# Kernel tuning notes

Measured on AMD Instinct MI355X. Metric: run time of the kernel, lower is better.

## Reference

```python
import jax, jax.numpy as jnp
import numpy as np

D_MODEL = 1024
NHEAD = 16
HEAD_DIM = D_MODEL // NHEAD
SF_THRESHOLD = 4.0
SF_LEVELS = 8
STEP = SF_THRESHOLD / SF_LEVELS  # quantization step of ScaleAndFireNeuron
EPS = 1e-6


def setup_inputs() -> dict:
    key = jax.random.key(0)
    ks = jax.random.split(key, 12)
    B, L, D = 2, 2048, D_MODEL
    s = 1.0 / np.sqrt(D)
    inp = {
        "x": jax.random.normal(ks[0], (B, L, D), dtype=jnp.float32),
        "wq": jax.random.normal(ks[1], (D, D), dtype=jnp.float32) * s,
        "bq": jnp.zeros((D,), dtype=jnp.float32),
        "wk": jax.random.normal(ks[2], (D, D), dtype=jnp.float32) * s,
        "bk": jnp.zeros((D,), dtype=jnp.float32),
        "wv": jax.random.normal(ks[3], (D, D), dtype=jnp.float32) * s,
        "bv": jnp.zeros((D,), dtype=jnp.float32),
        "wo": jax.random.normal(ks[4], (D, D), dtype=jnp.float32) * s,
        "bo": jnp.zeros((D,), dtype=jnp.float32),
        "gq": jnp.ones((HEAD_DIM,), dtype=jnp.float32),  # SpikingQKNorm gain (q)
        "gk": jnp.ones((HEAD_DIM,), dtype=jnp.float32),  # SpikingQKNorm gain (k)
    }
    return inp


def _rms_norm(t, g):
    # SpikingQKNorm: RMS normalization over head_dim with learned gain
    return t * jax.lax.rsqrt(jnp.mean(t * t, axis=-1, keepdims=True) + EPS) * g


def _sfn(t):
    # ScaleAndFireNeuron: T=1 multi-level spike quantization with straight-through estimator.
    # Levels are integer multiples of STEP, clipped to +/- SF_LEVELS.
    q = jnp.clip(jnp.round(t / STEP), -SF_LEVELS, SF_LEVELS) * STEP
    return t + jax.lax.stop_gradient(q - t)


def reference(x, wq, bq, wk, bk, wv, bv, wo, bo, gq, gk):
    B, L, D = x.shape
    H, Dh = NHEAD, HEAD_DIM
    scale = Dh ** -0.5

    def proj(w, b):
        return (x @ w.T + b).reshape(B, L, H, Dh).transpose(0, 2, 1, 3)  # [B,H,L,Dh]

    q = _sfn(_rms_norm(proj(wq, bq), gq))
    k = _sfn(_rms_norm(proj(wk, bk), gk))
    v = _sfn(proj(wv, bv))

    scores = jnp.einsum('bhqd,bhkd->bhqk', q, k) * scale  # [B,H,L,L]
    probs = jax.nn.softmax(scores, axis=-1)
    out = jnp.einsum('bhqk,bhkd->bhqd', probs, v)  # [B,H,L,Dh]
    out = out.transpose(0, 2, 1, 3).reshape(B, L, D)
    return out @ wo.T + bo
```

## Files before the change

### kernel.cpp

```cpp
#include <hip/hip_runtime.h>
#include <stdint.h>

#define D_MODEL 1024
#define NHEAD 16
#define HEAD_DIM 64
#define SEQ 2048
#define BATCH 2
#define MROWS (BATCH*SEQ)
#define KVBLK 64
#define KVTILES (SEQ/KVBLK)

typedef unsigned short u16;
typedef short bf16x8 __attribute__((ext_vector_type(8)));
typedef float f32x4 __attribute__((ext_vector_type(4)));
typedef float f32x16 __attribute__((ext_vector_type(16)));

__device__ inline float bf2f(u16 h){ return __uint_as_float(((unsigned)h)<<16); }
__device__ inline u16 f2bf(float x){
  unsigned u = __float_as_uint(x);
  unsigned r = (u + 0x7FFFu + ((u>>16)&1u)) >> 16;
  return (u16)r;
}

__device__ inline f32x4 mfma_bf16(bf16x8 a, bf16x8 b, f32x4 c){
  return __builtin_amdgcn_mfma_f32_16x16x32_bf16(a, b, c, 0, 0, 0);
}
__device__ inline f32x16 mfma32_bf16(bf16x8 a, bf16x8 b, f32x16 c){
  return __builtin_amdgcn_mfma_f32_32x32x16_bf16(a, b, c, 0, 0, 0);
}

__device__ inline void gld_lds16(const u16* g, u16* l){
  __builtin_amdgcn_global_load_lds(
      (const __attribute__((address_space(1))) void*)g,
      (__attribute__((address_space(3))) void*)l, 16, 0, 0);
}

__device__ inline int swz8(int row){ return (row ^ (row >> 3)) & 7; }

__device__ inline uint32_t pack_bf2(float p0, float p1){
  uint32_t u0 = __float_as_uint(p0) + 0x8000u;
  uint32_t u1 = __float_as_uint(p1) + 0x8000u;
  return __builtin_amdgcn_perm(u1, u0, 0x07060302u);
}

__global__ __launch_bounds__(256) void pack_split(const float* __restrict__ src,
                                                  u16* __restrict__ hi, u16* __restrict__ lo, int n4){
  int i = blockIdx.x*256 + threadIdx.x;
  if (i >= n4) return;
  float4 v = ((const float4*)src)[i];
  float vv[4] = {v.x, v.y, v.z, v.w};
  u16 h[4], l[4];
  #pragma unroll
  for (int j=0;j<4;j++){
    h[j] = f2bf(vv[j]);
    l[j] = f2bf(vv[j] - bf2f(h[j]));
  }
  ((ushort4*)hi)[i] = make_ushort4(h[0],h[1],h[2],h[3]);
  ((ushort4*)lo)[i] = make_ushort4(l[0],l[1],l[2],l[3]);
}

__global__ __launch_bounds__(256) void pack_bias(const float* __restrict__ bq, const float* __restrict__ bk,
                                                 const float* __restrict__ bv, float* __restrict__ out){
  int i = blockIdx.x*256 + threadIdx.x;
  if (i < 1024) out[i] = bq[i];
  else if (i < 2048) out[i] = bk[i-1024];
  else if (i < 3072) out[i] = bv[i-2048];
}

template<int PHASES, int MODE>
__global__ __launch_bounds__(256) void gemm_bt(
    const u16* __restrict__ a_hi, const u16* __restrict__ a_lo,
    const u16* __restrict__ b_hi, const u16* __restrict__ b_lo,
    const float* __restrict__ bias,
    float* __restrict__ out_f,
    u16* __restrict__ qb, u16* __restrict__ kb, u16* __restrict__ vb,
    const float* __restrict__ gq, const float* __restrict__ gk,
    int M, int N, int K)
{
  __shared__ u16 lds[2][8192];
  const int tid = threadIdx.x;
  const int lane = tid & 63;
  const int w = tid >> 6;
  const int wr = w >> 1, wc = w & 1;
  const int m0 = blockIdx.x * 128;
  const int n0 = blockIdx.y * 128;
  const int KS = K / 32;
  const int NT = PHASES * KS;

  f32x4 acc[4][4];
  #pragma unroll
  for (int i=0;i<4;i++)
    #pragma unroll
    for (int j=0;j<4;j++) acc[i][j] = (f32x4){0.f,0.f,0.f,0.f};

  auto stage = [&](int buf, int kt){
    int ph = (PHASES==1) ? 0 : (kt / KS);
    int kk = (PHASES==1 ? kt : (kt % KS)) * 32;
    const u16* As = (ph==1) ? a_lo : a_hi;
    const u16* Bs = (ph==2) ? b_lo : b_hi;
    u16* base = &lds[buf][0];
    #pragma unroll
    for (int r=0;r<2;r++){
      const u16* g = As + (size_t)(m0 + (tid>>2) + r*64)*K + kk + (tid&3)*8;
      gld_lds16(g, base + w*512 + r*2048);
    }
    #pragma unroll
    for (int r=0;r<2;r++){
      const u16* g = Bs + (size_t)(n0 + (tid>>2) + r*64)*K + kk + (tid&3)*8;
      gld_lds16(g, base + 4096 + w*512 + r*2048);
    }
  };

  auto compute = [&](int buf){
    const u16* la = &lds[buf][0];
    const u16* lb = &lds[buf][4096];
    const int koff = (lane>>4)*8;
    const int rowa = wr*64 + (lane&15);
    const int rowb = wc*64 + (lane&15);
    bf16x8 af[4], bfv[4];
    #pragma unroll
    for (int i=0;i<4;i++) af[i]  = *(const bf16x8*)&la[(rowa + i*16)*32 + koff];
    #pragma unroll
    for (int i=0;i<4;i++) bfv[i] = *(const bf16x8*)&lb[(rowb + i*16)*32 + koff];
    #pragma unroll
    for (int i=0;i<4;i++)
      #pragma unroll
      for (int j=0;j<4;j++)
        acc[i][j] = mfma_bf16(af[i], bfv[j], acc[i][j]);
  };

  stage(0, 0);
  for (int kt=0; kt<NT; ++kt){
    __syncthreads();
    if (kt+1 < NT) stage((kt+1)&1, kt+1);
    compute(kt&1);
  }

  const int gcolbase = n0 + wc*64;
  if (MODE == 0){
    #pragma unroll
    for (int j=0;j<4;j++){
      float bj = bias ? bias[gcolbase + j*16 + (lane&15)] : 0.f;
      #pragma unroll
      for (int i=0;i<4;i++){
        int row = m0 + wr*64 + i*16 + (lane>>4)*4;
        #pragma unroll
        for (int r=0;r<4;r++)
          out_f[(size_t)(row+r)*N + gcolbase + j*16 + (lane&15)] = acc[i][j][r] + bj;
      }
    }
  } else {
    const int sidx = gcolbase >> 6;
    const int ttype = sidx < 16 ? 0 : (sidx < 32 ? 1 : 2);
    u16* dst = ttype==0 ? qb : (ttype==1 ? kb : vb);
    const int h = sidx - (ttype==1 ? 16 : (ttype==2 ? 32 : 0));
    float gvals[4], bvals[4];
    #pragma unroll
    for (int j=0;j<4;j++){
      int dh = j*16 + (lane&15);
      bvals[j] = bias[gcolbase + dh];
      gvals[j] = ttype==0 ? gq[dh] : (ttype==1 ? gk[dh] : 1.0f);
    }
    #pragma unroll
    for (int i=0;i<4;i++){
      #pragma unroll
      for (int r=0;r<4;r++){
        float tv[4];
        float ssq = 0.f;
        #pragma unroll
        for (int j=0;j<4;j++){ tv[j] = acc[i][j][r] + bvals[j]; ssq += tv[j]*tv[j]; }
        ssq += __shfl_xor(ssq, 1);
        ssq += __shfl_xor(ssq, 2);
        ssq += __shfl_xor(ssq, 4);
        ssq += __shfl_xor(ssq, 8);
        float s = 1.0f;
        if (ttype < 2) s = 1.0f / sqrtf(ssq * (1.0f/64.0f) + 1e-6f);
        int row = m0 + wr*64 + i*16 + (lane>>4)*4 + r;
        int bi = row >> 11, li = row & 2047;
        size_t obase = ((size_t)(bi*NHEAD + h)*SEQ + li)*HEAD_DIM;
        #pragma unroll
        for (int j=0;j<4;j++){
          float val = tv[j] * s * gvals[j];
          float z = rintf(val * 2.0f);
          z = fminf(8.0f, fmaxf(-8.0f, z));
          dst[obase + j*16 + (lane&15)] = f2bf(z * 0.5f);
        }
      }
    }
  }
}

__global__ __launch_bounds__(256) void transpose_v(const u16* __restrict__ v, u16* __restrict__ vt){
  __shared__ u16 tl[64][66];
  int bh = blockIdx.x >> 5;
  int l0 = (blockIdx.x & 31) * 64;
  int tid = threadIdx.x;
  #pragma unroll
  for (int it=0; it<2; ++it){
    int idx = tid + it*256;
    int row = idx >> 3, g = idx & 7;
    bf16x8 d = *(const bf16x8*)(v + ((size_t)bh*SEQ + l0 + row)*64 + g*8);
    #pragma unroll
    for (int j=0;j<8;j++) tl[row][g*8+j] = (u16)d[j];
  }
  __syncthreads();
  #pragma unroll
  for (int it=0; it<2; ++it){
    int idx = tid + it*256;
    int dh = idx >> 3, g = idx & 7;
    u16 tmp[8];
    #pragma unroll
    for (int j=0;j<8;j++) tmp[j] = tl[g*8+j][dh];
    *(bf16x8*)(vt + ((size_t)bh*HEAD_DIM + dh)*SEQ + l0 + g*8) = *(const bf16x8*)tmp;
  }
}

__global__ __launch_bounds__(256) void attn_kernel(
    const u16* __restrict__ qb, const u16* __restrict__ kb, const u16* __restrict__ vt,
    u16* __restrict__ attn_out)
{
  __shared__ u16 lds_k[2][KVBLK*64];
  __shared__ u16 lds_v[2][64*KVBLK];
  const int tid = threadIdx.x, lane = tid & 63, w = tid >> 6;
  const int bh = blockIdx.y;
  const int q0 = blockIdx.x * 128;
  const size_t kvbase = (size_t)bh * SEQ * HEAD_DIM;
  const size_t vtbase = (size_t)bh * HEAD_DIM * SEQ;
  const int l31 = lane & 31, hi = lane >> 5;

  bf16x8 qf[4];
  #pragma unroll
  for (int kd=0; kd<4; kd++){
    const u16* g = qb + kvbase + (size_t)(q0 + w*32 + l31)*64 + kd*16 + hi*8;
    bf16x8 v = *(const bf16x8*)g;
    #pragma unroll
    for (int j=0;j<8;j++) ((u16*)&v)[j] = f2bf(bf2f((u16)v[j]) * 0.125f);
    qf[kd] = v;
  }

  float m_s = -3.0e38f, l_s = 0.f;
  f32x16 o0, o1;
  #pragma unroll
  for (int r=0;r<16;r++){ o0[r] = 0.f; o1[r] = 0.f; }

  auto stage = [&](int buf, int t){
    const int kv0 = t * KVBLK;
    #pragma unroll
    for (int r=0;r<2;r++){
      int idx = tid + r*256;
      int row = idx >> 3, grp = idx & 7;
      const u16* g = kb + kvbase + (size_t)(kv0 + row)*64 + ((grp ^ swz8(row))<<3);
      gld_lds16(g, &lds_k[buf][idx<<3]);
    }
    #pragma unroll
    for (int r=0;r<2;r++){
      int idx = tid + r*256;
      int row = idx >> 3, grp = idx & 7;
      const u16* g = vt + vtbase + (size_t)row*SEQ + kv0 + ((grp ^ swz8(row))<<3);
      gld_lds16(g, &lds_v[buf][idx<<3]);
    }
  };

  stage(0, 0);
  for (int t=0; t<KVTILES; ++t){
    __syncthreads();
    if (t+1 < KVTILES) stage((t+1)&1, t+1);
    const int buf = t & 1;

    f32x16 s0, s1;
    #pragma unroll
    for (int r=0;r<16;r++){ s0[r] = 0.f; s1[r] = 0.f; }
    __builtin_amdgcn_s_setprio(1);
    #pragma unroll
    for (int kd=0; kd<4; kd++){
      int row0 = l31;
      int row1 = 32 + l31;
      bf16x8 a0 = *(const bf16x8*)&lds_k[buf][row0*64 + (((kd*2+hi) ^ swz8(row0))<<3)];
      bf16x8 a1 = *(const bf16x8*)&lds_k[buf][row1*64 + (((kd*2+hi) ^ swz8(row1))<<3)];
      s0 = mfma32_bf16(a0, qf[kd], s0);
      s1 = mfma32_bf16(a1, qf[kd], s1);
    }
    __builtin_amdgcn_s_setprio(0);

    float pmax = s0[0];
    #pragma unroll
    for (int r=1;r<16;r++) pmax = fmaxf(pmax, s0[r]);
    #pragma unroll
    for (int r=0;r<16;r++) pmax = fmaxf(pmax, s1[r]);
    pmax = fmaxf(pmax, __shfl_xor(pmax, 32));

    if (__any(pmax - m_s > 8.0f)) {
      float mnew = fmaxf(m_s, pmax);
      float c = __expf(m_s - mnew);
      m_s = mnew;
      l_s *= c;
      #pragma unroll
      for (int r=0;r<16;r++){
        float cr = __shfl(c, (r&3) + 8*(r>>2) + 4*hi);
        o0[r] *= cr; o1[r] *= cr;
      }
    }

    float rsum = 0.f;
    #pragma unroll
    for (int r=0;r<16;r++){ float p = __expf(s0[r] - m_s); s0[r] = p; rsum += p; }
    #pragma unroll
    for (int r=0;r<16;r++){ float p = __expf(s1[r] - m_s); s1[r] = p; rsum += p; }
    rsum += __shfl_xor(rsum, 32);
    l_s += rsum;

    uint32_t W[2][4][2];
    #pragma unroll
    for (int g=0; g<4; g++){
      W[0][g][0] = pack_bf2(s0[g*4+0], s0[g*4+1]);
      W[0][g][1] = pack_bf2(s0[g*4+2], s0[g*4+3]);
      W[1][g][0] = pack_bf2(s1[g*4+0], s1[g*4+1]);
      W[1][g][1] = pack_bf2(s1[g*4+2], s1[g*4+3]);
    }
    bf16x8 pa[4];
    #pragma unroll
    for (int ks=0; ks<4; ks++){
      const int kvb = ks >> 1, ks0 = ks & 1;
      uint32_t own0 = hi ? W[kvb][ks0*2+1][0] : W[kvb][ks0*2][0];
      uint32_t own1 = hi ? W[kvb][ks0*2+1][1] : W[kvb][ks0*2][1];
      uint32_t t0   = hi ? W[kvb][ks0*2][0]   : W[kvb][ks0*2+1][0];
      uint32_t t1   = hi ? W[kvb][ks0*2][1]   : W[kvb][ks0*2+1][1];
      uint32_t sw0  = (uint32_t)__shfl_xor((int)t0, 32);
      uint32_t sw1  = (uint32_t)__shfl_xor((int)t1, 32);
      uint32_t words[4];
      words[0] = hi ? sw0 : own0;
      words[1] = hi ? sw1 : own1;
      words[2] = hi ? own0 : sw0;
      words[3] = hi ? own1 : sw1;
      pa[ks] = *(const bf16x8*)words;
    }

    __builtin_amdgcn_s_setprio(1);
    #pragma unroll
    for (int ks=0; ks<4; ks++){
      int row0 = l31;
      int row1 = 32 + l31;
      bf16x8 vb0 = *(const bf16x8*)&lds_v[buf][row0*64 + (((ks*2+hi) ^ swz8(row0))<<3)];
      bf16x8 vb1 = *(const bf16x8*)&lds_v[buf][row1*64 + (((ks*2+hi) ^ swz8(row1))<<3)];
      o0 = mfma32_bf16(pa[ks], vb0, o0);
      o1 = mfma32_bf16(pa[ks], vb1, o1);
    }
    __builtin_amdgcn_s_setprio(0);
  }

  const int b = bh >> 4, h = bh & 15;
  #pragma unroll
  for (int r=0;r<16;r++){
    int q = (r&3) + 8*(r>>2) + 4*hi;
    float linv = 1.0f / __shfl(l_s, q);
    int row = q0 + w*32 + q;
    size_t obase = ((size_t)b*SEQ + row)*D_MODEL + h*64;
    attn_out[obase + l31]      = f2bf(o0[r] * linv);
    attn_out[obase + 32 + l31] = f2bf(o1[r] * linv);
  }
}

extern "C" void kernel_launch(void* const* d_in, const int* in_sizes, int n_in,
                              void* d_out, int out_size, void* d_ws, size_t ws_size,
                              hipStream_t stream){
  const float* x  = (const float*)d_in[0];
  const float* wq = (const float*)d_in[1];
  const float* bq = (const float*)d_in[2];
  const float* wk = (const float*)d_in[3];
  const float* bk = (const float*)d_in[4];
  const float* wv = (const float*)d_in[5];
  const float* bv = (const float*)d_in[6];
  const float* wo = (const float*)d_in[7];
  const float* bo = (const float*)d_in[8];
  const float* gq = (const float*)d_in[9];
  const float* gk = (const float*)d_in[10];
  float* out = (float*)d_out;

  char* ws = (char*)d_ws;
  size_t off = 0;
  auto alloc = [&](size_t bytes) -> char* {
    char* p = ws + off; off += (bytes + 255) & ~(size_t)255; return p;
  };
  const size_t ND = (size_t)MROWS * D_MODEL;
  u16* x_hi    = (u16*)alloc(ND*2);
  u16* x_lo    = (u16*)alloc(ND*2);
  u16* wqkv_hi = (u16*)alloc((size_t)3072*1024*2);
  u16* wqkv_lo = (u16*)alloc((size_t)3072*1024*2);
  u16* wo_hi   = (u16*)alloc((size_t)1024*1024*2);
  u16* wo_lo   = (u16*)alloc((size_t)1024*1024*2);
  float* bqkv  = (float*)alloc(3072*4);
  u16* q_bf    = (u16*)alloc(ND*2);
  u16* k_bf    = (u16*)alloc(ND*2);
  u16* v_bf    = (u16*)alloc(ND*2);
  u16* vT      = (u16*)alloc(ND*2);
  u16* attn_bf = (u16*)alloc(ND*2);
  (void)ws_size; (void)in_sizes; (void)n_in; (void)out_size;

  pack_split<<<4096, 256, 0, stream>>>(x,  x_hi, x_lo, (int)(ND/4));
  pack_split<<<1024, 256, 0, stream>>>(wq, wqkv_hi,           wqkv_lo,           262144);
  pack_split<<<1024, 256, 0, stream>>>(wk, wqkv_hi + 1048576, wqkv_lo + 1048576, 262144);
  pack_split<<<1024, 256, 0, stream>>>(wv, wqkv_hi + 2097152, wqkv_lo + 2097152, 262144);
  pack_split<<<1024, 256, 0, stream>>>(wo, wo_hi, wo_lo, 262144);
  pack_bias<<<12, 256, 0, stream>>>(bq, bk, bv, bqkv);

  gemm_bt<3,1><<<dim3(32,24), 256, 0, stream>>>(x_hi, x_lo, wqkv_hi, wqkv_lo, bqkv,
        nullptr, q_bf, k_bf, v_bf, gq, gk, MROWS, 3072, 1024);

  transpose_v<<<1024, 256, 0, stream>>>(v_bf, vT);

  attn_kernel<<<dim3(16,32), 256, 0, stream>>>(q_bf, k_bf, vT, attn_bf);

  gemm_bt<1,0><<<dim3(32,8), 256, 0, stream>>>(attn_bf, nullptr, wo_hi, nullptr, bo,
        out, nullptr, nullptr, nullptr, nullptr, nullptr, MROWS, 1024, 1024);
}
```

Baseline: 193.3 us.

## Restructure QKV split-precision GEMM, double attention KV tile, merge weight packing

The QKV GEMM now uses a dedicated kernel. In its first 32 k-steps it stages A_hi, A_lo and B_hi together, so the B_hi fragment is reused for both hi and lo passes, which removes one full reload of B_hi. The attention kernel processes 128-key tiles as two 64-key halves, halving the number of barrier and staging iterations at the cost of larger LDS buffers that may lower occupancy. The four weight-packing launches are merged into one kernel to cut launch overhead.

Result: faster. 181.4 us (-6.1%).

```diff
diff --git a/kernel.cpp b/kernel.cpp
--- a/kernel.cpp
+++ b/kernel.cpp
@@ -7,7 +7,7 @@
 #define SEQ 2048
 #define BATCH 2
 #define MROWS (BATCH*SEQ)
-#define KVBLK 64
+#define KVBLK 128
 #define KVTILES (SEQ/KVBLK)
 
 typedef unsigned short u16;
@@ -59,6 +59,27 @@
   ((ushort4*)lo)[i] = make_ushort4(l[0],l[1],l[2],l[3]);
 }
 
+__global__ __launch_bounds__(256) void pack_w(const float* __restrict__ wq, const float* __restrict__ wk,
+                                              const float* __restrict__ wv, const float* __restrict__ wo,
+                                              u16* __restrict__ qkv_hi, u16* __restrict__ qkv_lo,
+                                              u16* __restrict__ wo_hi, u16* __restrict__ wo_lo){
+  int which = blockIdx.x >> 10;
+  int i = ((blockIdx.x & 1023) << 8) + threadIdx.x;
+  const float* src = which==0 ? wq : which==1 ? wk : which==2 ? wv : wo;
+  u16* hi = (which==3) ? wo_hi : qkv_hi + ((size_t)which << 20);
+  u16* lo = (which==3) ? wo_lo : qkv_lo + ((size_t)which << 20);
+  float4 v = ((const float4*)src)[i];
+  float vv[4] = {v.x, v.y, v.z, v.w};
+  u16 h[4], l[4];
+  #pragma unroll
+  for (int j=0;j<4;j++){
+    h[j] = f2bf(vv[j]);
+    l[j] = f2bf(vv[j] - bf2f(h[j]));
+  }
+  ((ushort4*)hi)[i] = make_ushort4(h[0],h[1],h[2],h[3]);
+  ((ushort4*)lo)[i] = make_ushort4(l[0],l[1],l[2],l[3]);
+}
+
 __global__ __launch_bounds__(256) void pack_bias(const float* __restrict__ bq, const float* __restrict__ bk,
                                                  const float* __restrict__ bv, float* __restrict__ out){
   int i = blockIdx.x*256 + threadIdx.x;
@@ -67,14 +88,139 @@
   else if (i < 3072) out[i] = bv[i-2048];
 }
 
-template<int PHASES, int MODE>
-__global__ __launch_bounds__(256) void gemm_bt(
+__global__ __launch_bounds__(256) void gemm_qkv(
     const u16* __restrict__ a_hi, const u16* __restrict__ a_lo,
     const u16* __restrict__ b_hi, const u16* __restrict__ b_lo,
     const float* __restrict__ bias,
-    float* __restrict__ out_f,
     u16* __restrict__ qb, u16* __restrict__ kb, u16* __restrict__ vb,
-    const float* __restrict__ gq, const float* __restrict__ gk,
+    const float* __restrict__ gq, const float* __restrict__ gk)
+{
+  __shared__ u16 lds[2][12288];
+  const int tid = threadIdx.x;
+  const int lane = tid & 63;
+  const int w = tid >> 6;
+  const int wr = w >> 1, wc = w & 1;
+  const int m0 = blockIdx.x * 128;
+  const int n0 = blockIdx.y * 128;
+  const int K = 1024;
+
+  f32x4 acc[4][4];
+  #pragma unroll
+  for (int i=0;i<4;i++)
+    #pragma unroll
+    for (int j=0;j<4;j++) acc[i][j] = (f32x4){0.f,0.f,0.f,0.f};
+
+  auto stage = [&](int buf, int kt){
+    u16* base = &lds[buf][0];
+    if (kt < 32){
+      int kk = kt << 5;
+      #pragma unroll
+      for (int r=0;r<2;r++){
+        const u16* g = a_hi + (size_t)(m0 + (tid>>2) + r*64)*K + kk + (tid&3)*8;
+        gld_lds16(g, base + w*512 + r*2048);
+      }
+      #pragma unroll
+      for (int r=0;r<2;r++){
+        const u16* g = a_lo + (size_t)(m0 + (tid>>2) + r*64)*K + kk + (tid&3)*8;
+        gld_lds16(g, base + 4096 + w*512 + r*2048);
+      }
+      #pragma unroll
+      for (int r=0;r<2;r++){
+        const u16* g = b_hi + (size_t)(n0 + (tid>>2) + r*64)*K + kk + (tid&3)*8;
+        gld_lds16(g, base + 8192 + w*512 + r*2048);
+      }
+    } else {
+      int kk = (kt-32) << 5;
+      #pragma unroll
+      for (int r=0;r<2;r++){
+        const u16* g = a_hi + (size_t)(m0 + (tid>>2) + r*64)*K + kk + (tid&3)*8;
+        gld_lds16(g, base + w*512 + r*2048);
+      }
+      #pragma unroll
+      for (int r=0;r<2;r++){
+        const u16* g = b_lo + (size_t)(n0 + (tid>>2) + r*64)*K + kk + (tid&3)*8;
+        gld_lds16(g, base + 8192 + w*512 + r*2048);
+      }
+    }
+  };
+
+  const int koff = (lane>>4)*8;
+  const int rowa = wr*64 + (lane&15);
+  const int rowb = wc*64 + (lane&15);
+
+  stage(0, 0);
+  for (int kt=0; kt<64; ++kt){
+    __syncthreads();
+    if (kt+1 < 64) stage((kt+1)&1, kt+1);
+    const u16* la = &lds[kt&1][0];
+    const u16* lb = &lds[kt&1][8192];
+    bf16x8 bfv[4];
+    #pragma unroll
+    for (int j=0;j<4;j++) bfv[j] = *(const bf16x8*)&lb[(rowb + j*16)*32 + koff];
+    bf16x8 af[4];
+    #pragma unroll
+    for (int i=0;i<4;i++) af[i] = *(const bf16x8*)&la[(rowa + i*16)*32 + koff];
+    #pragma unroll
+    for (int i=0;i<4;i++)
+      #pragma unroll
+      for (int j=0;j<4;j++)
+        acc[i][j] = mfma_bf16(af[i], bfv[j], acc[i][j]);
+    if (kt < 32){
+      const u16* ll = &lds[kt&1][4096];
+      bf16x8 al[4];
+      #pragma unroll
+      for (int i=0;i<4;i++) al[i] = *(const bf16x8*)&ll[(rowa + i*16)*32 + koff];
+      #pragma unroll
+      for (int i=0;i<4;i++)
+        #pragma unroll
+        for (int j=0;j<4;j++)
+          acc[i][j] = mfma_bf16(al[i], bfv[j], acc[i][j]);
+    }
+  }
+
+  const int gcolbase = n0 + wc*64;
+  const int sidx = gcolbase >> 6;
+  const int ttype = sidx < 16 ? 0 : (sidx < 32 ? 1 : 2);
+  u16* dst = ttype==0 ? qb : (ttype==1 ? kb : vb);
+  const int h = sidx - (ttype==1 ? 16 : (ttype==2 ? 32 : 0));
+  float gvals[4], bvals[4];
+  #pragma unroll
+  for (int j=0;j<4;j++){
+    int dh = j*16 + (lane&15);
+    bvals[j] = bias[gcolbase + dh];
+    gvals[j] = ttype==0 ? gq[dh] : (ttype==1 ? gk[dh] : 1.0f);
+  }
+  #pragma unroll
+  for (int i=0;i<4;i++){
+    #pragma unroll
+    for (int r=0;r<4;r++){
+      float tv[4];
+      float ssq = 0.f;
+      #pragma unroll
+      for (int j=0;j<4;j++){ tv[j] = acc[i][j][r] + bvals[j]; ssq += tv[j]*tv[j]; }
+      ssq += __shfl_xor(ssq, 1);
+      ssq += __shfl_xor(ssq, 2);
+      ssq += __shfl_xor(ssq, 4);
+      ssq += __shfl_xor(ssq, 8);
+      float s = 1.0f;
+      if (ttype < 2) s = 1.0f / sqrtf(ssq * (1.0f/64.0f) + 1e-6f);
+      int row = m0 + wr*64 + i*16 + (lane>>4)*4 + r;
+      int bi = row >> 11, li = row & 2047;
+      size_t obase = ((size_t)(bi*NHEAD + h)*SEQ + li)*HEAD_DIM;
+      #pragma unroll
+      for (int j=0;j<4;j++){
+        float val = tv[j] * s * gvals[j];
+        float z = rintf(val * 2.0f);
+        z = fminf(8.0f, fmaxf(-8.0f, z));
+        dst[obase + j*16 + (lane&15)] = f2bf(z * 0.5f);
+      }
+    }
+  }
+}
+
+__global__ __launch_bounds__(256) void gemm_bt(
+    const u16* __restrict__ a_hi, const u16* __restrict__ b_hi,
+    const float* __restrict__ bias, float* __restrict__ out_f,
     int M, int N, int K)
 {
   __shared__ u16 lds[2][8192];
@@ -84,8 +230,7 @@
   const int wr = w >> 1, wc = w & 1;
   const int m0 = blockIdx.x * 128;
   const int n0 = blockIdx.y * 128;
-  const int KS = K / 32;
-  const int NT = PHASES * KS;
+  const int NT = K / 32;
 
   f32x4 acc[4][4];
   #pragma unroll
@@ -94,26 +239,26 @@
     for (int j=0;j<4;j++) acc[i][j] = (f32x4){0.f,0.f,0.f,0.f};
 
   auto stage = [&](int buf, int kt){
-    int ph = (PHASES==1) ? 0 : (kt / KS);
-    int kk = (PHASES==1 ? kt : (kt % KS)) * 32;
-    const u16* As = (ph==1) ? a_lo : a_hi;
-    const u16* Bs = (ph==2) ? b_lo : b_hi;
+    int kk = kt * 32;
     u16* base = &lds[buf][0];
     #pragma unroll
     for (int r=0;r<2;r++){
-      const u16* g = As + (size_t)(m0 + (tid>>2) + r*64)*K + kk + (tid&3)*8;
+      const u16* g = a_hi + (size_t)(m0 + (tid>>2) + r*64)*K + kk + (tid&3)*8;
       gld_lds16(g, base + w*512 + r*2048);
     }
     #pragma unroll
     for (int r=0;r<2;r++){
-      const u16* g = Bs + (size_t)(n0 + (tid>>2) + r*64)*K + kk + (tid&3)*8;
+      const u16* g = b_hi + (size_t)(n0 + (tid>>2) + r*64)*K + kk + (tid&3)*8;
       gld_lds16(g, base + 4096 + w*512 + r*2048);
     }
   };
 
-  auto compute = [&](int buf){
-    const u16* la = &lds[buf][0];
-    const u16* lb = &lds[buf][4096];
+  stage(0, 0);
+  for (int kt=0; kt<NT; ++kt){
+    __syncthreads();
+    if (kt+1 < NT) stage((kt+1)&1, kt+1);
+    const u16* la = &lds[kt&1][0];
+    const u16* lb = &lds[kt&1][4096];
     const int koff = (lane>>4)*8;
     const int rowa = wr*64 + (lane&15);
     const int rowb = wc*64 + (lane&15);
@@ -127,65 +272,18 @@
       #pragma unroll
       for (int j=0;j<4;j++)
         acc[i][j] = mfma_bf16(af[i], bfv[j], acc[i][j]);
-  };
-
-  stage(0, 0);
-  for (int kt=0; kt<NT; ++kt){
-    __syncthreads();
-    if (kt+1 < NT) stage((kt+1)&1, kt+1);
-    compute(kt&1);
   }
 
   const int gcolbase = n0 + wc*64;
-  if (MODE == 0){
-    #pragma unroll
-    for (int j=0;j<4;j++){
-      float bj = bias ? bias[gcolbase + j*16 + (lane&15)] : 0.f;
-      #pragma unroll
-      for (int i=0;i<4;i++){
-        int row = m0 + wr*64 + i*16 + (lane>>4)*4;
-        #pragma unroll
-        for (int r=0;r<4;r++)
-          out_f[(size_t)(row+r)*N + gcolbase + j*16 + (lane&15)] = acc[i][j][r] + bj;
-      }
-    }
-  } else {
-    const int sidx = gcolbase >> 6;
-    const int ttype = sidx < 16 ? 0 : (sidx < 32 ? 1 : 2);
-    u16* dst = ttype==0 ? qb : (ttype==1 ? kb : vb);
-    const int h = sidx - (ttype==1 ? 16 : (ttype==2 ? 32 : 0));
-    float gvals[4], bvals[4];
-    #pragma unroll
-    for (int j=0;j<4;j++){
-      int dh = j*16 + (lane&15);
-      bvals[j] = bias[gcolbase + dh];
-      gvals[j] = ttype==0 ? gq[dh] : (ttype==1 ? gk[dh] : 1.0f);
-    }
+  #pragma unroll
+  for (int j=0;j<4;j++){
+    float bj = bias[gcolbase + j*16 + (lane&15)];
     #pragma unroll
     for (int i=0;i<4;i++){
-      #pragma unroll
-      for (int r=0;r<4;r++){
-        float tv[4];
-        float ssq = 0.f;
-        #pragma unroll
-        for (int j=0;j<4;j++){ tv[j] = acc[i][j][r] + bvals[j]; ssq += tv[j]*tv[j]; }
-        ssq += __shfl_xor(ssq, 1);
-        ssq += __shfl_xor(ssq, 2);
-        ssq += __shfl_xor(ssq, 4);
-        ssq += __shfl_xor(ssq, 8);
-        float s = 1.0f;
-        if (ttype < 2) s = 1.0f / sqrtf(ssq * (1.0f/64.0f) + 1e-6f);
-        int row = m0 + wr*64 + i*16 + (lane>>4)*4 + r;
-        int bi = row >> 11, li = row & 2047;
-        size_t obase = ((size_t)(bi*NHEAD + h)*SEQ + li)*HEAD_DIM;
-        #pragma unroll
-        for (int j=0;j<4;j++){
-          float val = tv[j] * s * gvals[j];
-          float z = rintf(val * 2.0f);
-          z = fminf(8.0f, fmaxf(-8.0f, z));
-          dst[obase + j*16 + (lane&15)] = f2bf(z * 0.5f);
-        }
-      }
+      int row = m0 + wr*64 + i*16 + (lane>>4)*4;
+      #pragma unroll
+      for (int r=0;r<4;r++)
+        out_f[(size_t)(row+r)*N + gcolbase + j*16 + (lane&15)] = acc[i][j][r] + bj;
     }
   }
 }
@@ -246,16 +344,16 @@
   auto stage = [&](int buf, int t){
     const int kv0 = t * KVBLK;
     #pragma unroll
-    for (int r=0;r<2;r++){
+    for (int r=0;r<4;r++){
       int idx = tid + r*256;
       int row = idx >> 3, grp = idx & 7;
       const u16* g = kb + kvbase + (size_t)(kv0 + row)*64 + ((grp ^ swz8(row))<<3);
       gld_lds16(g, &lds_k[buf][idx<<3]);
     }
     #pragma unroll
-    for (int r=0;r<2;r++){
+    for (int r=0;r<4;r++){
       int idx = tid + r*256;
-      int row = idx >> 3, grp = idx & 7;
+      int row = idx >> 4, grp = idx & 15;
       const u16* g = vt + vtbase + (size_t)row*SEQ + kv0 + ((grp ^ swz8(row))<<3);
       gld_lds16(g, &lds_v[buf][idx<<3]);
     }
@@ -267,85 +365,88 @@
     if (t+1 < KVTILES) stage((t+1)&1, t+1);
     const int buf = t & 1;
 
-    f32x16 s0, s1;
-    #pragma unroll
-    for (int r=0;r<16;r++){ s0[r] = 0.f; s1[r] = 0.f; }
-    __builtin_amdgcn_s_setprio(1);
-    #pragma unroll
-    for (int kd=0; kd<4; kd++){
-      int row0 = l31;
-      int row1 = 32 + l31;
-      bf16x8 a0 = *(const bf16x8*)&lds_k[buf][row0*64 + (((kd*2+hi) ^ swz8(row0))<<3)];
-      bf16x8 a1 = *(const bf16x8*)&lds_k[buf][row1*64 + (((kd*2+hi) ^ swz8(row1))<<3)];
-      s0 = mfma32_bf16(a0, qf[kd], s0);
-      s1 = mfma32_bf16(a1, qf[kd], s1);
-    }
-    __builtin_amdgcn_s_setprio(0);
-
-    float pmax = s0[0];
-    #pragma unroll
-    for (int r=1;r<16;r++) pmax = fmaxf(pmax, s0[r]);
-    #pragma unroll
-    for (int r=0;r<16;r++) pmax = fmaxf(pmax, s1[r]);
-    pmax = fmaxf(pmax, __shfl_xor(pmax, 32));
-
-    if (__any(pmax - m_s > 8.0f)) {
-      float mnew = fmaxf(m_s, pmax);
-      float c = __expf(m_s - mnew);
-      m_s = mnew;
-      l_s *= c;
-      #pragma unroll
-      for (int r=0;r<16;r++){
-        float cr = __shfl(c, (r&3) + 8*(r>>2) + 4*hi);
-        o0[r] *= cr; o1[r] *= cr;
-      }
-    }
-
-    float rsum = 0.f;
-    #pragma unroll
-    for (int r=0;r<16;r++){ float p = __expf(s0[r] - m_s); s0[r] = p; rsum += p; }
-    #pragma unroll
-    for (int r=0;r<16;r++){ float p = __expf(s1[r] - m_s); s1[r] = p; rsum += p; }
-    rsum += __shfl_xor(rsum, 32);
-    l_s += rsum;
-
-    uint32_t W[2][4][2];
-    #pragma unroll
-    for (int g=0; g<4; g++){
-      W[0][g][0] = pack_bf2(s0[g*4+0], s0[g*4+1]);
-      W[0][g][1] = pack_bf2(s0[g*4+2], s0[g*4+3]);
-      W[1][g][0] = pack_bf2(s1[g*4+0], s1[g*4+1]);
-      W[1][g][1] = pack_bf2(s1[g*4+2], s1[g*4+3]);
-    }
-    bf16x8 pa[4];
-    #pragma unroll
-    for (int ks=0; ks<4; ks++){
-      const int kvb = ks >> 1, ks0 = ks & 1;
-      uint32_t own0 = hi ? W[kvb][ks0*2+1][0] : W[kvb][ks0*2][0];
-      uint32_t own1 = hi ? W[kvb][ks0*2+1][1] : W[kvb][ks0*2][1];
-      uint32_t t0   = hi ? W[kvb][ks0*2][0]   : W[kvb][ks0*2+1][0];
-      uint32_t t1   = hi ? W[kvb][ks0*2][1]   : W[kvb][ks0*2+1][1];
-      uint32_t sw0  = (uint32_t)__shfl_xor((int)t0, 32);
-      uint32_t sw1  = (uint32_t)__shfl_xor((int)t1, 32);
-      uint32_t words[4];
-      words[0] = hi ? sw0 : own0;
-      words[1] = hi ? sw1 : own1;
-      words[2] = hi ? own0 : sw0;
-      words[3] = hi ? own1 : sw1;
-      pa[ks] = *(const bf16x8*)words;
-    }
-
-    __builtin_amdgcn_s_setprio(1);
-    #pragma unroll
-    for (int ks=0; ks<4; ks++){
-      int row0 = l31;
-      int row1 = 32 + l31;
-      bf16x8 vb0 = *(const bf16x8*)&lds_v[buf][row0*64 + (((ks*2+hi) ^ swz8(row0))<<3)];
-      bf16x8 vb1 = *(const bf16x8*)&lds_v[buf][row1*64 + (((ks*2+hi) ^ swz8(row1))<<3)];
-      o0 = mfma32_bf16(pa[ks], vb0, o0);
-      o1 = mfma32_bf16(pa[ks], vb1, o1);
-    }
-    __builtin_amdgcn_s_setprio(0);
+    #pragma unroll
+    for (int half=0; half<2; ++half){
+      f32x16 s0, s1;
+      #pragma unroll
+      for (int r=0;r<16;r++){ s0[r] = 0.f; s1[r] = 0.f; }
+      const int row0 = half*64 + l31;
+      const int row1 = half*64 + 32 + l31;
+      __builtin_amdgcn_s_setprio(1);
+      #pragma unroll
+      for (int kd=0; kd<4; kd++){
+        bf16x8 a0 = *(const bf16x8*)&lds_k[buf][row0*64 + (((kd*2+hi) ^ swz8(row0))<<3)];
+        bf16x8 a1 = *(const bf16x8*)&lds_k[buf][row1*64 + (((kd*2+hi) ^ swz8(row1))<<3)];
+        s0 = mfma32_bf16(a0, qf[kd], s0);
+        s1 = mfma32_bf16(a1, qf[kd], s1);
+      }
+      __builtin_amdgcn_s_setprio(0);
+
+      float pmax = s0[0];
+      #pragma unroll
+      for (int r=1;r<16;r++) pmax = fmaxf(pmax, s0[r]);
+      #pragma unroll
+      for (int r=0;r<16;r++) pmax = fmaxf(pmax, s1[r]);
+      pmax = fmaxf(pmax, __shfl_xor(pmax, 32));
+
+      if (__any(pmax - m_s > 8.0f)) {
+        float mnew = fmaxf(m_s, pmax);
+        float c = __expf(m_s - mnew);
+        m_s = mnew;
+        l_s *= c;
+        #pragma unroll
+        for (int r=0;r<16;r++){
+          float cr = __shfl(c, (r&3) + 8*(r>>2) + 4*hi);
+          o0[r] *= cr; o1[r] *= cr;
+        }
+      }
+
+      float rsum = 0.f;
+      #pragma unroll
+      for (int r=0;r<16;r++){ float p = __expf(s0[r] - m_s); s0[r] = p; rsum += p; }
+      #pragma unroll
+      for (int r=0;r<16;r++){ float p = __expf(s1[r] - m_s); s1[r] = p; rsum += p; }
+      rsum += __shfl_xor(rsum, 32);
+      l_s += rsum;
+
+      uint32_t W[2][4][2];
+      #pragma unroll
+      for (int g=0; g<4; g++){
+        W[0][g][0] = pack_bf2(s0[g*4+0], s0[g*4+1]);
+        W[0][g][1] = pack_bf2(s0[g*4+2], s0[g*4+3]);
+        W[1][g][0] = pack_bf2(s1[g*4+0], s1[g*4+1]);
+        W[1][g][1] = pack_bf2(s1[g*4+2], s1[g*4+3]);
+      }
+      bf16x8 pa[4];
+      #pragma unroll
+      for (int ks=0; ks<4; ks++){
+        const int kvb = ks >> 1, ks0 = ks & 1;
+        uint32_t own0 = hi ? W[kvb][ks0*2+1][0] : W[kvb][ks0*2][0];
+        uint32_t own1 = hi ? W[kvb][ks0*2+1][1] : W[kvb][ks0*2][1];
+        uint32_t t0   = hi ? W[kvb][ks0*2][0]   : W[kvb][ks0*2+1][0];
+        uint32_t t1   = hi ? W[kvb][ks0*2][1]   : W[kvb][ks0*2+1][1];
+        uint32_t sw0  = (uint32_t)__shfl_xor((int)t0, 32);
+        uint32_t sw1  = (uint32_t)__shfl_xor((int)t1, 32);
+        uint32_t words[4];
+        words[0] = hi ? sw0 : own0;
+        words[1] = hi ? sw1 : own1;
+        words[2] = hi ? own0 : sw0;
+        words[3] = hi ? own1 : sw1;
+        pa[ks] = *(const bf16x8*)words;
+      }
+
+      __builtin_amdgcn_s_setprio(1);
+      #pragma unroll
+      for (int ks=0; ks<4; ks++){
+        const int rv0 = l31, rv1 = 32 + l31;
+        const int cg = half*8 + ks*2 + hi;
+        bf16x8 vb0 = *(const bf16x8*)&lds_v[buf][rv0*KVBLK + ((cg ^ swz8(rv0))<<3)];
+        bf16x8 vb1 = *(const bf16x8*)&lds_v[buf][rv1*KVBLK + ((cg ^ swz8(rv1))<<3)];
+        o0 = mfma32_bf16(pa[ks], vb0, o0);
+        o1 = mfma32_bf16(pa[ks], vb1, o1);
+      }
+      __builtin_amdgcn_s_setprio(0);
+    }
   }
 
   const int b = bh >> 4, h = bh & 15;
@@ -396,20 +497,16 @@
   u16* attn_bf = (u16*)alloc(ND*2);
   (void)ws_size; (void)in_sizes; (void)n_in; (void)out_size;
 
-  pack_split<<<4096, 256, 0, stream>>>(x,  x_hi, x_lo, (int)(ND/4));
-  pack_split<<<1024, 256, 0, stream>>>(wq, wqkv_hi,           wqkv_lo,           262144);
-  pack_split<<<1024, 256, 0, stream>>>(wk, wqkv_hi + 1048576, wqkv_lo + 1048576, 262144);
-  pack_split<<<1024, 256, 0, stream>>>(wv, wqkv_hi + 2097152, wqkv_lo + 2097152, 262144);
-  pack_split<<<1024, 256, 0, stream>>>(wo, wo_hi, wo_lo, 262144);
+  pack_split<<<4096, 256, 0, stream>>>(x, x_hi, x_lo, (int)(ND/4));
+  pack_w<<<4096, 256, 0, stream>>>(wq, wk, wv, wo, wqkv_hi, wqkv_lo, wo_hi, wo_lo);
   pack_bias<<<12, 256, 0, stream>>>(bq, bk, bv, bqkv);
 
-  gemm_bt<3,1><<<dim3(32,24), 256, 0, stream>>>(x_hi, x_lo, wqkv_hi, wqkv_lo, bqkv,
-        nullptr, q_bf, k_bf, v_bf, gq, gk, MROWS, 3072, 1024);
+  gemm_qkv<<<dim3(32,24), 256, 0, stream>>>(x_hi, x_lo, wqkv_hi, wqkv_lo, bqkv,
+        q_bf, k_bf, v_bf, gq, gk);
 
   transpose_v<<<1024, 256, 0, stream>>>(v_bf, vT);
 
   attn_kernel<<<dim3(16,32), 256, 0, stream>>>(q_bf, k_bf, vT, attn_bf);
 
-  gemm_bt<1,0><<<dim3(32,8), 256, 0, stream>>>(attn_bf, nullptr, wo_hi, nullptr, bo,
-        out, nullptr, nullptr, nullptr, nullptr, nullptr, MROWS, 1024, 1024);
-}
+  gemm_bt<<<dim3(32,8), 256, 0, stream>>>(attn_bf, wo_hi, bo, out, MROWS, 1024, 1024);
+}
```
